# Performance work log

Hardware: AMD Instinct MI355X
Metric: run time of the kernel (lower is better)

Reference implementation:

```python
import jax, jax.numpy as jnp
import numpy as np

NUM_ANCHORS = 3
NUM_CLASSES = 80
STRIDES = (16.0, 32.0)
ANCHORS = (
    jnp.array([[12.64, 19.39], [37.88, 51.48], [55.71, 138.31]], dtype=jnp.float32),
    jnp.array([[126.91, 78.23], [131.57, 214.55], [279.92, 258.87]], dtype=jnp.float32),
)


def conv1x1(x, w, b):
    # x: [B,C,H,W], w: [O,C], b: [O] -> [B,O,H,W]
    return jnp.einsum('bchw,oc->bohw', x, w) + b[None, :, None, None]


def decode_level(reg, obj, cls, stride, anchors):
    # reg: [B,12,H,W], obj: [B,3,H,W], cls: [B,80,H,W]
    B, _, H, W = reg.shape
    r = reg.transpose(0, 2, 3, 1).reshape(B, H, W, NUM_ANCHORS, 4)
    o = obj.transpose(0, 2, 3, 1).reshape(B, H, W, NUM_ANCHORS, 1)
    c = cls.transpose(0, 2, 3, 1)[:, :, :, None, :]  # [B,H,W,1,80], shared across anchors
    gy, gx = jnp.meshgrid(jnp.arange(H, dtype=reg.dtype), jnp.arange(W, dtype=reg.dtype), indexing='ij')
    grid = jnp.stack([gx, gy], axis=-1)[None, :, :, None, :]  # [1,H,W,1,2] = (x, y)
    xy = (jax.nn.sigmoid(r[..., :2]) * 2.0 - 0.5 + grid) * stride
    wh = (jax.nn.sigmoid(r[..., 2:4]) * 2.0) ** 2 * anchors  # anchors [3,2] broadcast
    ob = jax.nn.sigmoid(o)
    cp = jnp.broadcast_to(jax.nn.softmax(c, axis=-1), (B, H, W, NUM_ANCHORS, NUM_CLASSES))
    boxes = jnp.concatenate([xy, wh, ob, cp], axis=-1)  # [B,H,W,3,85]
    return boxes.reshape(B, H * W * NUM_ANCHORS, 5 + NUM_CLASSES)


def setup_inputs() -> dict:
    key = jax.random.key(0)
    ks = jax.random.split(key, 12)
    B, C = 64, 72
    inp = {
        'feat_reg0': jax.random.normal(ks[0], (B, C, 40, 40), jnp.float32),
        'feat_obj0': jax.random.normal(ks[1], (B, C, 40, 40), jnp.float32),
        'feat_cls0': jax.random.normal(ks[2], (B, C, 40, 40), jnp.float32),
        'feat_reg1': jax.random.normal(ks[3], (B, C, 20, 20), jnp.float32),
        'feat_obj1': jax.random.normal(ks[4], (B, C, 20, 20), jnp.float32),
        'feat_cls1': jax.random.normal(ks[5], (B, C, 20, 20), jnp.float32),
        'w_reg': jax.random.normal(ks[6], (4 * NUM_ANCHORS, C), jnp.float32) * 0.05,
        'b_reg': jax.random.normal(ks[7], (4 * NUM_ANCHORS,), jnp.float32) * 0.05,
        'w_obj': jax.random.normal(ks[8], (NUM_ANCHORS, C), jnp.float32) * 0.05,
        'b_obj': jax.random.normal(ks[9], (NUM_ANCHORS,), jnp.float32) * 0.05,
        'w_cls': jax.random.normal(ks[10], (NUM_CLASSES, C), jnp.float32) * 0.05,
        'b_cls': jax.random.normal(ks[11], (NUM_CLASSES,), jnp.float32) * 0.05,
    }
    return inp


def reference(feat_reg0, feat_obj0, feat_cls0, feat_reg1, feat_obj1, feat_cls1,
              w_reg, b_reg, w_obj, b_obj, w_cls, b_cls):
    feats = ((feat_reg0, feat_obj0, feat_cls0), (feat_reg1, feat_obj1, feat_cls1))
    outs = []
    for i, (fr, fo, fc) in enumerate(feats):
        reg = conv1x1(fr, w_reg, b_reg)
        obj = conv1x1(fo, w_obj, b_obj)
        cls = conv1x1(fc, w_cls, b_cls)
        outs.append(decode_level(reg, obj, cls, STRIDES[i], ANCHORS[i]))
    return jnp.concatenate(outs, axis=1)  # [B, 6000, 85]
```

## Files before the change

### kernel.cpp

```cpp
#include <hip/hip_runtime.h>
#include <math.h>

#define BLOCK 256
#define NPOS 64
#define C_IN 72
#define AST 100
#define RST 100
#define NFRAG 21

typedef short short8  __attribute__((ext_vector_type(8)));
typedef float floatx4 __attribute__((ext_vector_type(4)));

__device__ __forceinline__ unsigned short f2bf(float f) {
    unsigned u = __float_as_uint(f);
    u += 0x7FFFu + ((u >> 16) & 1u);
    return (unsigned short)(u >> 16);
}
__device__ __forceinline__ float sigf(float x) {
    return __builtin_amdgcn_rcpf(1.0f + __expf(-x));
}

__global__ void __launch_bounds__(BLOCK)
build_bfrags_kernel(const float* __restrict__ w_reg,
                    const float* __restrict__ w_obj,
                    const float* __restrict__ w_cls,
                    short8* __restrict__ frags)
{
    int idx = blockIdx.x * BLOCK + threadIdx.x;
    if (idx >= NFRAG * 64) return;
    int lane = idx & 63;
    int fi   = idx >> 6;
    int tile = fi / 3, kc = fi - tile * 3;
    int m = lane & 15, quad = lane >> 4;
    const float* wrow;
    bool valid = true;
    if (tile == 0)      { wrow = w_reg + m * C_IN; valid = (m < 12); }
    else if (tile == 1) { wrow = w_obj + m * C_IN; valid = (m < 3); }
    else                { wrow = w_cls + ((tile - 2) * 16 + m) * C_IN; }
    short8 r = {0, 0, 0, 0, 0, 0, 0, 0};
    if (valid && !(kc == 2 && quad != 0)) {
        const float* p = wrow + kc * 32 + quad * 8;
#pragma unroll
        for (int j = 0; j < 8; ++j) r[j] = (short)f2bf(p[j]);
    }
    frags[fi * 64 + lane] = r;
}

__global__ void __launch_bounds__(BLOCK, 4)
yolo_head_kernel(const float* __restrict__ fr0, const float* __restrict__ fo0, const float* __restrict__ fc0,
                 const float* __restrict__ fr1, const float* __restrict__ fo1, const float* __restrict__ fc1,
                 const float* __restrict__ b_reg, const float* __restrict__ b_obj,
                 const float* __restrict__ b_cls,
                 const short8* __restrict__ wfrag,
                 float* __restrict__ out)
{
    __shared__ __align__(16) short sA[3 * NPOS * AST];
    __shared__ int itab[255];
    float* row = (float*)sA;

    const int bid  = blockIdx.x;
    const int tid  = threadIdx.x;
    const int lane = tid & 63;
    const int wv   = tid >> 6;
    const int m    = lane & 15;
    const int quad = lane >> 4;

    if (tid < 255) {
        int k  = tid;
        int a  = (k >= 85) + (k >= 170);
        int kk = k - a * 85;
        int idx = (kk < 5) ? (a * 5 + kk) : (kk + 11);
        itab[k] = (idx << 1) | (kk >= 5);
    }

    int lvl, b, pos0, HW, W, LO;
    const float *fr, *fo, *fc;
    if (bid < 1600) {
        lvl = 0; b = bid / 25; pos0 = (bid % 25) * NPOS;
        HW = 1600; W = 40; LO = 0; fr = fr0; fo = fo0; fc = fc0;
    } else {
        int t = bid - 1600;
        lvl = 1; b = t / 7; pos0 = (t % 7) * NPOS;
        HW = 400; W = 20; LO = 4800; fr = fr1; fo = fo1; fc = fc1;
    }
    const float STRIDE = lvl ? 32.0f : 16.0f;
    const int active = (HW - pos0 < NPOS) ? (HW - pos0) : NPOS;
    const int pos    = pos0 + lane;
    const int posc   = (pos < HW) ? pos : (HW - 1);

    {
        int* sAi = (int*)sA;
        const float* srcs[3] = {fr, fo, fc};
#pragma unroll
        for (int t = 0; t < 3; ++t) {
            const float* sp = srcs[t] + b * C_IN * HW + posc;
            int* dp = sAi + t * (NPOS * AST / 2) + lane * (AST / 2);
#pragma unroll
            for (int i = 0; i < 9; ++i) {
                int c0 = wv * 2 + i * 8;
                float v0 = sp[c0 * HW];
                float v1 = sp[(c0 + 1) * HW];
                dp[c0 >> 1] = (int)f2bf(v0) | ((int)f2bf(v1) << 16);
            }
        }
        for (int i = tid; i < 3 * NPOS * 12; i += BLOCK) {
            int t = i / (NPOS * 12), r = i - t * (NPOS * 12);
            int p = r / 12, s = r - p * 12;
            sAi[t * (NPOS * AST / 2) + p * (AST / 2) + 36 + s] = 0;
        }
    }

    short8 bf[NFRAG];
#pragma unroll
    for (int i = 0; i < NFRAG; ++i) bf[i] = wfrag[i * 64 + lane];

    __syncthreads();

    const int mt = wv;
    auto afrag = [&](int t, int kc) -> short8 {
        return *reinterpret_cast<const short8*>(
            sA + t * (NPOS * AST) + (mt * 16 + m) * AST + kc * 32 + quad * 8);
    };

    floatx4 accR = {0, 0, 0, 0}, accO = {0, 0, 0, 0}, accC[5];
#pragma unroll
    for (int kc = 0; kc < 3; ++kc)
        accR = __builtin_amdgcn_mfma_f32_16x16x32_bf16(afrag(0, kc), bf[0 * 3 + kc], accR, 0, 0, 0);
#pragma unroll
    for (int kc = 0; kc < 3; ++kc)
        accO = __builtin_amdgcn_mfma_f32_16x16x32_bf16(afrag(1, kc), bf[1 * 3 + kc], accO, 0, 0, 0);
#pragma unroll
    for (int nt = 0; nt < 5; ++nt) {
        floatx4 a4 = {0, 0, 0, 0};
#pragma unroll
        for (int kc = 0; kc < 3; ++kc)
            a4 = __builtin_amdgcn_mfma_f32_16x16x32_bf16(afrag(2, kc), bf[(nt + 2) * 3 + kc], a4, 0, 0, 0);
        accC[nt] = a4;
    }

    __syncthreads();

#pragma unroll
    for (int i = 0; i < 4; ++i) {
        int pl = mt * 16 + quad * 4 + i;
        if (m < 12) row[pl * RST + m]      = accR[i] + b_reg[m];
        if (m < 3)  row[pl * RST + 12 + m] = accO[i] + b_obj[m];
    }
#pragma unroll
    for (int nt = 0; nt < 5; ++nt) {
        float bc = b_cls[nt * 16 + m];
#pragma unroll
        for (int i = 0; i < 4; ++i) {
            int pl = mt * 16 + quad * 4 + i;
            row[pl * RST + 16 + nt * 16 + m] = __expf(accC[nt][i] + bc);
        }
    }
    __syncthreads();

    if (tid < NPOS) {
        float* rr = row + tid * RST;
        float s = 0.f;
#pragma unroll
        for (int i2 = 0; i2 < 20; ++i2) {
            floatx4 e4 = *reinterpret_cast<const floatx4*>(rr + 16 + i2 * 4);
            s += (e4[0] + e4[1]) + (e4[2] + e4[3]);
        }
        rr[99] = __builtin_amdgcn_rcpf(s);

        float r12[12], ob3[3];
#pragma unroll
        for (int j = 0; j < 12; ++j) r12[j] = rr[j];
#pragma unroll
        for (int a = 0; a < 3; ++a) ob3[a] = rr[12 + a];

        int pg = pos0 + tid; if (pg >= HW) pg = HW - 1;
        const int gyi = lvl ? (pg / 20) : (pg / 40);
        const float gx = (float)(pg - gyi * W);
        const float gy = (float)gyi;
        float A[6];
        if (lvl == 0) { A[0]=12.64f;  A[1]=19.39f;  A[2]=37.88f;  A[3]=51.48f;  A[4]=55.71f;  A[5]=138.31f; }
        else          { A[0]=126.91f; A[1]=78.23f;  A[2]=131.57f; A[3]=214.55f; A[4]=279.92f; A[5]=258.87f; }
#pragma unroll
        for (int a = 0; a < 3; ++a) {
            float x  = (sigf(r12[4*a + 0]) * 2.0f - 0.5f + gx) * STRIDE;
            float y  = (sigf(r12[4*a + 1]) * 2.0f - 0.5f + gy) * STRIDE;
            float tw = sigf(r12[4*a + 2]) * 2.0f;
            float th = sigf(r12[4*a + 3]) * 2.0f;
            rr[a*5 + 0] = x;
            rr[a*5 + 1] = y;
            rr[a*5 + 2] = tw * tw * A[2*a + 0];
            rr[a*5 + 3] = th * th * A[2*a + 1];
            rr[a*5 + 4] = sigf(ob3[a]);
        }
    }
    __syncthreads();

    const int limit = active * 255;
    float* outp = out + (b * 510000 + LO * 85 + pos0 * 255);

    for (int f0 = tid * 4; f0 < limit; f0 += BLOCK * 4) {
        float4 v4;
        float* pv = &v4.x;
#pragma unroll
        for (int j = 0; j < 4; ++j) {
            int ff = f0 + j;
            int op = ff / 255;
            int k  = ff - op * 255;
            int t  = itab[k];
            const float* rw = row + op * RST;
            float v = rw[t >> 1];
            if (t & 1) v *= rw[99];
            pv[j] = v;
        }
        *reinterpret_cast<float4*>(outp + f0) = v4;
    }
}

extern "C" void kernel_launch(void* const* d_in, const int* in_sizes, int n_in,
                              void* d_out, int out_size, void* d_ws, size_t ws_size,
                              hipStream_t stream) {
    (void)in_sizes; (void)n_in; (void)ws_size; (void)out_size;
    const float* fr0  = (const float*)d_in[0];
    const float* fo0  = (const float*)d_in[1];
    const float* fc0  = (const float*)d_in[2];
    const float* fr1  = (const float*)d_in[3];
    const float* fo1  = (const float*)d_in[4];
    const float* fc1  = (const float*)d_in[5];
    const float* wreg = (const float*)d_in[6];
    const float* breg = (const float*)d_in[7];
    const float* wobj = (const float*)d_in[8];
    const float* bobj = (const float*)d_in[9];
    const float* wcls = (const float*)d_in[10];
    const float* bcls = (const float*)d_in[11];
    float* out = (float*)d_out;
    short8* frags = (short8*)d_ws;

    build_bfrags_kernel<<<6, BLOCK, 0, stream>>>(wreg, wobj, wcls, frags);

    yolo_head_kernel<<<2048, BLOCK, 0, stream>>>(
        fr0, fo0, fc0, fr1, fo1, fc1,
        breg, bobj, bcls, frags, out);
}
```

Before: 253.3 us.

## Batch feature loads before bf16 packing, pad LDS stride, write output per-row

Feature loads are grouped into a register array and held with asm barriers so all global reads issue before any packing, and the weight-fragment loads are moved ahead of them so they overlap. The LDS A-tile stride is padded from 100 to 102 shorts, which may reduce bank conflicts on the MFMA fragment reads. The class-exp row layout is compacted so the reciprocal sum sits at index 95. The output store loop changes from float4 writes using a shared index table to per-wavefront, per-position scalar coalesced writes with lane-computed indices, which removes the itab table and the divisions. Launch bounds drop from 4 to 3 waves per SIMD to allow the extra registers, at some cost in occupancy.

```diff
diff --git a/kernel.cpp b/kernel.cpp
--- a/kernel.cpp
+++ b/kernel.cpp
@@ -4,7 +4,9 @@
 #define BLOCK 256
 #define NPOS 64
 #define C_IN 72
-#define AST 100
+#define AST 102
+#define ASTI 51
+#define TSZ (NPOS * AST)
 #define RST 100
 #define NFRAG 21
 
@@ -46,7 +48,7 @@
     frags[fi * 64 + lane] = r;
 }
 
-__global__ void __launch_bounds__(BLOCK, 4)
+__global__ void __launch_bounds__(BLOCK, 3)
 yolo_head_kernel(const float* __restrict__ fr0, const float* __restrict__ fo0, const float* __restrict__ fc0,
                  const float* __restrict__ fr1, const float* __restrict__ fo1, const float* __restrict__ fc1,
                  const float* __restrict__ b_reg, const float* __restrict__ b_obj,
@@ -54,8 +56,7 @@
                  const short8* __restrict__ wfrag,
                  float* __restrict__ out)
 {
-    __shared__ __align__(16) short sA[3 * NPOS * AST];
-    __shared__ int itab[255];
+    __shared__ __align__(16) short sA[3 * TSZ];
     float* row = (float*)sA;
 
     const int bid  = blockIdx.x;
@@ -64,14 +65,6 @@
     const int wv   = tid >> 6;
     const int m    = lane & 15;
     const int quad = lane >> 4;
-
-    if (tid < 255) {
-        int k  = tid;
-        int a  = (k >= 85) + (k >= 170);
-        int kk = k - a * 85;
-        int idx = (kk < 5) ? (a * 5 + kk) : (kk + 11);
-        itab[k] = (idx << 1) | (kk >= 5);
-    }
 
     int lvl, b, pos0, HW, W, LO;
     const float *fr, *fo, *fc;
@@ -88,38 +81,48 @@
     const int pos    = pos0 + lane;
     const int posc   = (pos < HW) ? pos : (HW - 1);
 
+    short8 bf[NFRAG];
+#pragma unroll
+    for (int i = 0; i < NFRAG; ++i) bf[i] = wfrag[i * 64 + lane];
+
     {
         int* sAi = (int*)sA;
         const float* srcs[3] = {fr, fo, fc};
 #pragma unroll
         for (int t = 0; t < 3; ++t) {
             const float* sp = srcs[t] + b * C_IN * HW + posc;
-            int* dp = sAi + t * (NPOS * AST / 2) + lane * (AST / 2);
+            int* dp = sAi + t * (TSZ / 2) + lane * ASTI;
+            float lf[18];
 #pragma unroll
             for (int i = 0; i < 9; ++i) {
                 int c0 = wv * 2 + i * 8;
-                float v0 = sp[c0 * HW];
-                float v1 = sp[(c0 + 1) * HW];
-                dp[c0 >> 1] = (int)f2bf(v0) | ((int)f2bf(v1) << 16);
+                lf[2 * i]     = sp[c0 * HW];
+                lf[2 * i + 1] = sp[(c0 + 1) * HW];
             }
-        }
-        for (int i = tid; i < 3 * NPOS * 12; i += BLOCK) {
-            int t = i / (NPOS * 12), r = i - t * (NPOS * 12);
-            int p = r / 12, s = r - p * 12;
-            sAi[t * (NPOS * AST / 2) + p * (AST / 2) + 36 + s] = 0;
-        }
-    }
-
-    short8 bf[NFRAG];
-#pragma unroll
-    for (int i = 0; i < NFRAG; ++i) bf[i] = wfrag[i * 64 + lane];
-
+#pragma unroll
+            for (int i = 0; i < 18; ++i)
+                asm volatile("" : "+v"(lf[i]));
+#pragma unroll
+            for (int i = 0; i < 9; ++i) {
+                int c0 = wv * 2 + i * 8;
+                dp[c0 >> 1] = (int)f2bf(lf[2 * i]) | ((int)f2bf(lf[2 * i + 1]) << 16);
+            }
+        }
+#pragma unroll
+        for (int i = 0; i < NFRAG; ++i)
+            asm volatile("" : "+v"(*(floatx4*)&bf[i]));
+        for (int i = tid; i < 3 * NPOS * 15; i += BLOCK) {
+            int t = i / (NPOS * 15), r = i - t * (NPOS * 15);
+            int p = r / 15, s = r - p * 15;
+            sAi[t * (TSZ / 2) + p * ASTI + 36 + s] = 0;
+        }
+    }
     __syncthreads();
 
     const int mt = wv;
     auto afrag = [&](int t, int kc) -> short8 {
         return *reinterpret_cast<const short8*>(
-            sA + t * (NPOS * AST) + (mt * 16 + m) * AST + kc * 32 + quad * 8);
+            sA + t * TSZ + (mt * 16 + m) * AST + kc * 32 + quad * 8);
     };
 
     floatx4 accR = {0, 0, 0, 0}, accO = {0, 0, 0, 0}, accC[5];
@@ -152,20 +155,20 @@
 #pragma unroll
         for (int i = 0; i < 4; ++i) {
             int pl = mt * 16 + quad * 4 + i;
-            row[pl * RST + 16 + nt * 16 + m] = __expf(accC[nt][i] + bc);
+            row[pl * RST + 15 + nt * 16 + m] = __expf(accC[nt][i] + bc);
         }
     }
     __syncthreads();
 
     if (tid < NPOS) {
         float* rr = row + tid * RST;
-        float s = 0.f;
-#pragma unroll
-        for (int i2 = 0; i2 < 20; ++i2) {
-            floatx4 e4 = *reinterpret_cast<const floatx4*>(rr + 16 + i2 * 4);
+        float s = rr[15] + rr[92] + rr[93] + rr[94];
+#pragma unroll
+        for (int i2 = 4; i2 < 23; ++i2) {
+            floatx4 e4 = *reinterpret_cast<const floatx4*>(rr + i2 * 4);
             s += (e4[0] + e4[1]) + (e4[2] + e4[3]);
         }
-        rr[99] = __builtin_amdgcn_rcpf(s);
+        rr[95] = __builtin_amdgcn_rcpf(s);
 
         float r12[12], ob3[3];
 #pragma unroll
@@ -195,24 +198,30 @@
     }
     __syncthreads();
 
-    const int limit = active * 255;
+    int wi[4], wflag[4];
+#pragma unroll
+    for (int j = 0; j < 4; ++j) {
+        int f = lane + 64 * j;
+        int k = (f > 254) ? 0 : f;
+        int a  = (k >= 85) + (k >= 170);
+        int kk = k - a * 85;
+        wi[j]    = (kk < 5) ? (a * 5 + kk) : (15 + (kk - 5));
+        wflag[j] = (kk >= 5);
+    }
     float* outp = out + (b * 510000 + LO * 85 + pos0 * 255);
 
-    for (int f0 = tid * 4; f0 < limit; f0 += BLOCK * 4) {
-        float4 v4;
-        float* pv = &v4.x;
+    for (int p = wv; p < active; p += 4) {
+        const float* rr = row + p * RST;
+        float inv = rr[95];
+        float* po = outp + p * 255 + lane;
 #pragma unroll
         for (int j = 0; j < 4; ++j) {
-            int ff = f0 + j;
-            int op = ff / 255;
-            int k  = ff - op * 255;
-            int t  = itab[k];
-            const float* rw = row + op * RST;
-            float v = rw[t >> 1];
-            if (t & 1) v *= rw[99];
-            pv[j] = v;
-        }
-        *reinterpret_cast<float4*>(outp + f0) = v4;
+            if (!(lane == 63 && j == 3)) {
+                float v = rr[wi[j]];
+                if (wflag[j]) v *= inv;
+                po[64 * j] = v;
+            }
+        }
     }
 }
 
```

Result: no change. 248.9 us (-1.7%).
